# Performance work log

Measured on AMD Instinct MI355X. Metric: run time of the kernel, lower is better.

The kernel has to match this reference:

```python
import jax, jax.numpy as jnp
import numpy as np
from jax import lax

B, T, IN = 32, 512, 32
SNN, TS, HID, HOR = 128, 4, 128, 96
K = 3
THR = 1.0
EPS = 1e-5


def _spike(x):
    # heaviside: fires when (mem - threshold) > 0
    return (x > 0).astype(x.dtype)


def _lif_scan(xs, beta, thr):
    """snntorch Leaky (reset_mechanism='subtract'): mem_t = beta*mem_{t-1} + x_t - spk_{t-1}*thr; spk_t = H(mem_t - thr).
    xs: (S, B, C); beta: (C,). Returns spikes (S,B,C) and membrane (S,B,C)."""
    def step(carry, x):
        mem, rst = carry
        mem = beta * mem + x - rst * thr
        spk = _spike(mem - thr)
        return (mem, lax.stop_gradient(spk)), (spk, mem)
    z = jnp.zeros(xs.shape[1:], xs.dtype)
    _, (spks, mems) = lax.scan(step, (z, z), xs)
    return spks, mems


def setup_inputs() -> dict:
    key = jax.random.key(0)
    ks = jax.random.split(key, 10)
    def rn(k, shape, scale=0.05):
        return jax.random.normal(k, shape, dtype=jnp.float32) * scale
    return {
        "x": jax.random.normal(ks[0], (B, T, IN), dtype=jnp.float32),
        "conv_w": rn(ks[1], (SNN * TS, IN, K)),
        "conv_b": jnp.zeros((SNN * TS,), jnp.float32),
        "bn1_g": jnp.ones((SNN * TS,), jnp.float32),
        "bn1_b": jnp.zeros((SNN * TS,), jnp.float32),
        "beta1": jnp.full((SNN,), 0.9, jnp.float32),
        "bn2_g": jnp.ones((SNN,), jnp.float32),
        "bn2_b": jnp.zeros((SNN,), jnp.float32),
        "beta2": jnp.full((SNN,), 0.9, jnp.float32),
        "gru_wih": rn(ks[2], (3 * HID, IN + SNN)),
        "gru_whh": rn(ks[3], (3 * HID, HID)),
        "gru_bih": jnp.zeros((3 * HID,), jnp.float32),
        "gru_bhh": jnp.zeros((3 * HID,), jnp.float32),
        "q_w": rn(ks[4], (HID, HID)), "q_b": jnp.zeros((HID,), jnp.float32),
        "k_w": rn(ks[5], (HID, HID)), "k_b": jnp.zeros((HID,), jnp.float32),
        "v_w": rn(ks[6], (HID, HID)), "v_b": jnp.zeros((HID,), jnp.float32),
        "bn3_g": jnp.ones((HID,), jnp.float32),
        "bn3_b": jnp.zeros((HID,), jnp.float32),
        "head_w": rn(ks[7], (HOR, HID)),
        "head_b": jnp.zeros((HOR,), jnp.float32),
    }


def reference(x, conv_w, conv_b, bn1_g, bn1_b, beta1, bn2_g, bn2_b, beta2,
              gru_wih, gru_whh, gru_bih, gru_bhh, q_w, q_b, k_w, k_b, v_w, v_b,
              bn3_g, bn3_b, head_w, head_b):
    beta1 = jnp.clip(beta1, 0.0, 0.99)
    beta2 = jnp.clip(beta2, 0.0, 0.99)
    # --- ConvSpikeEncoder: Conv1d -> BatchNorm1d (training stats) -> LIF scan ---
    h = lax.conv_general_dilated(x.transpose(0, 2, 1), conv_w, (1,), [(K // 2, K // 2)],
                                 dimension_numbers=('NCH', 'OIH', 'NCH'))
    h = h + conv_b[None, :, None]  # (B, SNN*TS, T)
    m = h.mean((0, 2), keepdims=True)
    v = jnp.var(h, (0, 2), keepdims=True)
    h = (h - m) * lax.rsqrt(v + EPS) * bn1_g[None, :, None] + bn1_b[None, :, None]
    # (B, SNN*TS, T) -> (T*TS, B, SNN), step index = t*TS + s
    h = h.transpose(0, 2, 1).reshape(B, T * TS, SNN).transpose(1, 0, 2)
    spk_enc, _ = _lif_scan(h, beta1, THR)  # (T*TS, B, SNN)
    # --- per-step BatchNorm1d over batch dim, then second LIF ---
    m2 = spk_enc.mean(1, keepdims=True)
    v2 = jnp.var(spk_enc, 1, keepdims=True)
    h2 = (spk_enc - m2) * lax.rsqrt(v2 + EPS) * bn2_g + bn2_b
    _, mem_rec = _lif_scan(h2, beta2, THR)  # (T*TS, B, SNN)
    # --- downsample membrane: mean over TS sub-steps ---
    mem_down = mem_rec.transpose(1, 0, 2).reshape(B, T, TS, SNN).mean(2)  # (B, T, SNN)
    hc = jnp.concatenate([x, mem_down], -1)  # (B, T, IN+SNN)
    # --- GRU (PyTorch gate order r,z,n) ---
    def gstep(hprev, xt):
        gi = xt @ gru_wih.T + gru_bih
        gh = hprev @ gru_whh.T + gru_bhh
        ir, iz, inn = jnp.split(gi, 3, -1)
        hr, hz, hn = jnp.split(gh, 3, -1)
        r = jax.nn.sigmoid(ir + hr)
        zg = jax.nn.sigmoid(iz + hz)
        n = jnp.tanh(inn + r * hn)
        hnew = (1.0 - zg) * n + zg * hprev
        return hnew, hnew
    _, gru_seq = lax.scan(gstep, jnp.zeros((B, HID), x.dtype), hc.transpose(1, 0, 2))
    g = gru_seq.transpose(1, 0, 2)  # (B, T, HID)
    # --- SpikingAttention: sigmoid(QK^T*scale) @ V, mean over T, BatchNorm ---
    Q = g @ q_w.T + q_b
    Kk = g @ k_w.T + k_b
    V = g @ v_w.T + v_b
    attn = jax.nn.sigmoid(jnp.einsum('btc,bsc->bts', Q, Kk) * (HID ** -0.5))
    out = jnp.einsum('bts,bsc->btc', attn, V).mean(1)  # (B, HID)
    m3 = out.mean(0, keepdims=True)
    v3 = jnp.var(out, 0, keepdims=True)
    out = (out - m3) * lax.rsqrt(v3 + EPS) * bn3_g + bn3_b
    return out @ head_w.T + head_b  # (B, HOR)
```

## Files before the change

kernel.cpp:

```cpp
#include <hip/hip_runtime.h>
#include <math.h>

#define EPSV 1e-5f

#if __has_builtin(__builtin_amdgcn_exp2f)
#define EXP2F(x) __builtin_amdgcn_exp2f(x)
#else
#define EXP2F(x) exp2f(x)
#endif
#if __has_builtin(__builtin_amdgcn_rcpf)
#define RCPF(x) __builtin_amdgcn_rcpf(x)
#else
#define RCPF(x) (1.0f/(x))
#endif

__device__ __forceinline__ float fsigmoid(float x){
  return RCPF(1.0f + EXP2F(-1.4426950408889634f * x));
}
__device__ __forceinline__ float ftanh(float x){
  return RCPF(0.5f + 0.5f * EXP2F(-2.8853900817779268f * x)) - 1.0f;
}
__device__ __forceinline__ unsigned short f2bf(float f){
  unsigned u = __float_as_uint(f);
  return (unsigned short)((u + 0x7FFFu + ((u >> 16) & 1u)) >> 16);
}

typedef __attribute__((ext_vector_type(8))) short bf16x8;
typedef __attribute__((ext_vector_type(8))) short s16x8;
typedef __attribute__((ext_vector_type(4))) float f32x4;
typedef __attribute__((ext_vector_type(2))) _Float16 f16x2;
typedef __attribute__((ext_vector_type(8))) _Float16 f16x8;

#if __has_builtin(__builtin_amdgcn_fdot2)
#define FDOT2(a,b,c) __builtin_amdgcn_fdot2(a,b,c,false)
#else
__device__ __forceinline__ float FDOT2(f16x2 a, f16x2 b, float c){
  return c + (float)a[0]*(float)b[0] + (float)a[1]*(float)b[1];
}
#endif

__device__ __forceinline__ float dot8(f16x8 w, f16x8 h, float acc){
  f16x2 w0 = {w[0],w[1]}, w1 = {w[2],w[3]}, w2 = {w[4],w[5]}, w3 = {w[6],w[7]};
  f16x2 h0 = {h[0],h[1]}, h1 = {h[2],h[3]}, h2 = {h[4],h[5]}, h3 = {h[6],h[7]};
  acc = FDOT2(w0,h0,acc); acc = FDOT2(w1,h1,acc);
  acc = FDOT2(w2,h2,acc); acc = FDOT2(w3,h3,acc);
  return acc;
}

__global__ __launch_bounds__(256) void k_conv(const float* __restrict__ x, const float* __restrict__ w,
        const float* __restrict__ cb, float* __restrict__ hp, float* __restrict__ s1g, float* __restrict__ s2g,
        unsigned short* __restrict__ x_bf){
  __shared__ float xs[32*321];
  __shared__ float ws[32*97];
  __shared__ float bs[32];
  const int tid = threadIdx.x;
  const int t0 = blockIdx.x * 8;
  const int n0 = blockIdx.y * 8;
  for (int idx = tid; idx < 32*10*32; idx += 256){
    int bq = idx / 320; int rem = idx - bq*320; int tt = rem >> 5; int i = rem & 31;
    int tg = t0 - 1 + tt;
    float v = 0.f;
    if (tg >= 0 && tg < 512) v = x[(bq*512 + tg)*32 + i];
    xs[bq*321 + tt*32 + i] = v;
  }
  for (int idx = tid; idx < 32*96; idx += 256){
    int row = idx / 96; int within = idx - row*96;
    int ss = row >> 3; int nl = row & 7;
    int c = ss*128 + n0 + nl;
    ws[row*97 + within] = w[c*96 + within];
  }
  if (tid < 32){
    int ss = tid >> 3, nl = tid & 7;
    bs[tid] = cb[ss*128 + n0 + nl];
  }
  __syncthreads();
  if (blockIdx.y == 0){
    for (int idx = tid; idx < 32*8*32; idx += 256){
      int bq = idx >> 8; int rem = idx & 255; int tt = rem >> 5; int i = rem & 31;
      x_bf[(bq*512 + t0 + tt)*32 + i] = f2bf(xs[bq*321 + (tt+1)*32 + i]);
    }
  }
  const int b = tid & 31;
  const int nl = tid >> 5;
  float acc[4][8];
  #pragma unroll
  for (int ss = 0; ss < 4; ++ss){
    float bv = bs[ss*8 + nl];
    #pragma unroll
    for (int t = 0; t < 8; ++t) acc[ss][t] = bv;
  }
  for (int i = 0; i < 32; ++i){
    #pragma unroll
    for (int k = 0; k < 3; ++k){
      float w0 = ws[(0*8+nl)*97 + i*3 + k];
      float w1 = ws[(1*8+nl)*97 + i*3 + k];
      float w2 = ws[(2*8+nl)*97 + i*3 + k];
      float w3 = ws[(3*8+nl)*97 + i*3 + k];
      #pragma unroll
      for (int t = 0; t < 8; ++t){
        float xv = xs[b*321 + (t+k)*32 + i];
        acc[0][t] += xv*w0; acc[1][t] += xv*w1; acc[2][t] += xv*w2; acc[3][t] += xv*w3;
      }
    }
  }
  #pragma unroll
  for (int ss = 0; ss < 4; ++ss){
    int n = n0 + nl;
    float s1 = 0.f, s2 = 0.f;
    #pragma unroll
    for (int t = 0; t < 8; ++t){
      float v = acc[ss][t];
      int s = (t0 + t)*4 + ss;
      hp[s*4096 + n*32 + b] = v;
      s1 += v; s2 += v*v;
    }
    #pragma unroll
    for (int off = 1; off < 32; off <<= 1){
      s1 += __shfl_xor(s1, off);
      s2 += __shfl_xor(s2, off);
    }
    if (b == 0){
      int c = ss*128 + n;
      atomicAdd(&s1g[c], s1);
      atomicAdd(&s2g[c], s2);
    }
  }
}

__global__ void k_bn1(const float* __restrict__ s1g, const float* __restrict__ s2g,
                      const float* __restrict__ g, const float* __restrict__ bb,
                      float* __restrict__ a1, float* __restrict__ b1){
  int c = threadIdx.x;
  float m = s1g[c] * (1.f/16384.f);
  float v = s2g[c] * (1.f/16384.f) - m*m;
  float sc = g[c] * rsqrtf(v + EPSV);
  a1[c] = sc;
  b1[c] = bb[c] - m*sc;
}

__global__ __launch_bounds__(256) void k_cvt_all(const float* __restrict__ wih,
        const float* __restrict__ qw, const float* __restrict__ kw, const float* __restrict__ vw,
        const float* __restrict__ whh,
        unsigned short* __restrict__ wih_bf, unsigned short* __restrict__ wqkv_bf,
        _Float16* __restrict__ whh_h){
  int i = blockIdx.x*256 + threadIdx.x;
  if (i < 61440){ wih_bf[i] = f2bf(wih[i]); return; }
  int r = i - 61440;
  if (r < 16384){ wqkv_bf[r] = f2bf(qw[r]); return; }
  r -= 16384;
  if (r < 16384){ wqkv_bf[16384 + r] = f2bf(kw[r]); return; }
  r -= 16384;
  if (r < 16384){ wqkv_bf[32768 + r] = f2bf(vw[r]); return; }
  r -= 16384;
  if (r < 49152){ whh_h[r] = (_Float16)whh[r]; }
}

__global__ __launch_bounds__(256) void k_lif(const float* __restrict__ hp,
        const float* __restrict__ a1, const float* __restrict__ b1,
        const float* __restrict__ beta1, const float* __restrict__ g2v, const float* __restrict__ b2v,
        const float* __restrict__ beta2, unsigned short* __restrict__ md_t){
  const int tid = threadIdx.x;
  const int b = tid & 31;
  const int n = blockIdx.x * 8 + (tid >> 5);
  float a1r0 = a1[0*128+n], a1r1 = a1[1*128+n], a1r2 = a1[2*128+n], a1r3 = a1[3*128+n];
  float b1r0 = b1[0*128+n], b1r1 = b1[1*128+n], b1r2 = b1[2*128+n], b1r3 = b1[3*128+n];
  float be1 = fminf(fmaxf(beta1[n], 0.f), 0.99f);
  float be2 = fminf(fmaxf(beta2[n], 0.f), 0.99f);
  float g2 = g2v[n], bb2 = b2v[n];
  float m1 = 0.f, r1 = 0.f, m2 = 0.f, r2 = 0.f;
  const float* base = hp + n*32 + b;
  float c0 = base[0], c1 = base[4096], c2 = base[2*4096], c3 = base[3*4096];
  const float* nb1 = base + 16384;
  float d0 = nb1[0], d1 = nb1[4096], d2 = nb1[2*4096], d3 = nb1[3*4096];

#define LIF_STEP(CV, A1R, B1R) { \
    float x1 = CV*A1R + B1R; \
    m1 = be1*m1 + x1 - r1; \
    bool sp = (m1 > 1.0f); \
    unsigned long long mk = __ballot(sp); \
    float spk = sp ? 1.f : 0.f; r1 = spk; \
    unsigned hf = (tid & 32) ? (unsigned)(mk >> 32) : (unsigned)mk; \
    float mean = (float)__popc(hf) * 0.03125f; \
    float var = mean - mean*mean; \
    float h2 = (spk - mean) * rsqrtf(var + EPSV) * g2 + bb2; \
    m2 = be2*m2 + h2 - r2; \
    r2 = (m2 > 1.0f) ? 1.f : 0.f; \
    accd += m2; }

  for (int t = 0; t < 512; ++t){
    float e0 = 0.f, e1 = 0.f, e2 = 0.f, e3 = 0.f;
    if (t < 510){
      const float* nb = base + (size_t)(t+2)*16384;
      e0 = nb[0]; e1 = nb[4096]; e2 = nb[2*4096]; e3 = nb[3*4096];
    }
    float accd = 0.f;
    LIF_STEP(c0, a1r0, b1r0)
    LIF_STEP(c1, a1r1, b1r1)
    LIF_STEP(c2, a1r2, b1r2)
    LIF_STEP(c3, a1r3, b1r3)
    md_t[((t*128) + n)*32 + b] = f2bf(accd * 0.25f);
    c0 = d0; c1 = d1; c2 = d2; c3 = d3;
    d0 = e0; d1 = e1; d2 = e2; d3 = e3;
  }
#undef LIF_STEP
}

__global__ __launch_bounds__(256) void k_tr(const unsigned short* __restrict__ md_t,
        unsigned short* __restrict__ md_bf){
  __shared__ unsigned short l[128][40];
  const int t = blockIdx.x;
  const int tid = threadIdx.x;
  const unsigned short* src = md_t + (size_t)t*4096;
  #pragma unroll
  for (int r = 0; r < 2; ++r){
    int idx = tid*16 + r*8;
    s16x8 v = *(const s16x8*)(src + idx);
    int nn = idx >> 5, b0 = idx & 31;
    #pragma unroll
    for (int e = 0; e < 8; ++e) l[nn][b0 + e] = (unsigned short)v[e];
  }
  __syncthreads();
  const int b = tid >> 3, seg = tid & 7;
  unsigned short tmp[16];
  #pragma unroll
  for (int i = 0; i < 16; ++i) tmp[i] = l[seg*16 + i][b];
  unsigned short* dst = md_bf + (size_t)(b*512 + t)*128 + seg*16;
  *(s16x8*)(dst + 0) = *(s16x8*)&tmp[0];
  *(s16x8*)(dst + 8) = *(s16x8*)&tmp[8];
}

__global__ __launch_bounds__(256) void k_mm_gi(const unsigned short* __restrict__ xbf,
        const unsigned short* __restrict__ mdbf, const unsigned short* __restrict__ wihbf,
        const float* __restrict__ bih, float* __restrict__ gi2){
  const int tid = threadIdx.x;
  const int w = tid >> 6, l = tid & 63;
  const int c16 = l & 15, kg = l >> 4;
  const int m0 = (blockIdx.x*4 + w) * 16;
  const int mrow = m0 + c16;
  bf16x8 a0 = *(const bf16x8*)&xbf[(size_t)mrow*32 + kg*8];
  const unsigned short* mdp = &mdbf[(size_t)mrow*128 + kg*8];
  bf16x8 a1 = *(const bf16x8*)(mdp + 0);
  bf16x8 a2 = *(const bf16x8*)(mdp + 32);
  bf16x8 a3 = *(const bf16x8*)(mdp + 64);
  bf16x8 a4 = *(const bf16x8*)(mdp + 96);
  for (int nt = 0; nt < 24; ++nt){
    int n0 = nt*16;
    const unsigned short* wp = &wihbf[(size_t)(n0 + c16)*160 + kg*8];
    bf16x8 b0 = *(const bf16x8*)(wp + 0);
    bf16x8 b1 = *(const bf16x8*)(wp + 32);
    bf16x8 b2 = *(const bf16x8*)(wp + 64);
    bf16x8 b3 = *(const bf16x8*)(wp + 96);
    bf16x8 b4 = *(const bf16x8*)(wp + 128);
    f32x4 acc = {0.f,0.f,0.f,0.f};
    acc = __builtin_amdgcn_mfma_f32_16x16x32_bf16(a0, b0, acc, 0, 0, 0);
    acc = __builtin_amdgcn_mfma_f32_16x16x32_bf16(a1, b1, acc, 0, 0, 0);
    acc = __builtin_amdgcn_mfma_f32_16x16x32_bf16(a2, b2, acc, 0, 0, 0);
    acc = __builtin_amdgcn_mfma_f32_16x16x32_bf16(a3, b3, acc, 0, 0, 0);
    acc = __builtin_amdgcn_mfma_f32_16x16x32_bf16(a4, b4, acc, 0, 0, 0);
    int n = n0 + c16;
    int gate = n >> 7;
    int jj = n & 127;
    float bias = bih[n];
    #pragma unroll
    for (int r = 0; r < 4; ++r){
      gi2[(size_t)(m0 + kg*4 + r)*512 + jj*4 + gate] = acc[r] + bias;
    }
  }
}

template<int SEL>
__device__ __forceinline__ float dpp_qp(float x){
  return __int_as_float(__builtin_amdgcn_mov_dpp(__float_as_int(x), SEL, 0xF, 0xF, true));
}
__device__ __forceinline__ float qbc(float x, int u){
  switch(u){
    case 0: return dpp_qp<0x00>(x);
    case 1: return dpp_qp<0x55>(x);
    case 2: return dpp_qp<0xAA>(x);
    default: return dpp_qp<0xFF>(x);
  }
}
__global__ __launch_bounds__(512, 2) void k_gru(const float* __restrict__ gi2, const _Float16* __restrict__ whh_h,
        const float* __restrict__ bhh, unsigned short* __restrict__ gout_bf){
  const int b = blockIdx.x;
  const int tid = threadIdx.x;
  const int j = tid >> 2;
  const int q = tid & 3;
  __shared__ _Float16 hs[2][144];
  const _Float16* wbr = whh_h + (size_t)(      j)*128 + q*32;
  const _Float16* wbz = whh_h + (size_t)(128 + j)*128 + q*32;
  const _Float16* wbn = whh_h + (size_t)(256 + j)*128 + q*32;
  f16x8 wr0 = *(const f16x8*)(wbr+ 0), wr1 = *(const f16x8*)(wbr+ 8),
        wr2 = *(const f16x8*)(wbr+16), wr3 = *(const f16x8*)(wbr+24);
  f16x8 wz0 = *(const f16x8*)(wbz+ 0), wz1 = *(const f16x8*)(wbz+ 8),
        wz2 = *(const f16x8*)(wbz+16), wz3 = *(const f16x8*)(wbz+24);
  f16x8 wn0 = *(const f16x8*)(wbn+ 0), wn1 = *(const f16x8*)(wbn+ 8),
        wn2 = *(const f16x8*)(wbn+16), wn3 = *(const f16x8*)(wbn+24);
  float bh_r = 0.f, bh_z = 0.f, bh_n = 0.f;
  if (!q){
    bh_r = bhh[j]; bh_z = bhh[128+j]; bh_n = bhh[256+j];
  }
  const float* gib = gi2 + (size_t)b*512*512;
  f32x4 G = *(const f32x4*)(gib + (size_t)q*512 + j*4);
  if (tid < 128) hs[0][tid] = (_Float16)0.f;
  float hprev = 0.f;
  __syncthreads();
  for (int g = 0; g < 128; ++g){
    f32x4 N = {0.f,0.f,0.f,0.f};
    if (g < 127) N = *(const f32x4*)(gib + (size_t)(4*(g+1) + q)*512 + j*4);
    #pragma unroll
    for (int u = 0; u < 4; ++u){
      const int t = g*4 + u;
      float gr = qbc(G[0], u);
      float gz = qbc(G[1], u);
      float gn = qbc(G[2], u);
      const f16x8* hq = (const f16x8*)&hs[t & 1][q*32];
      f16x8 h0 = hq[0], h1 = hq[1], h2 = hq[2], h3 = hq[3];
      float ar = 0.f, az = 0.f, an = 0.f;
      ar = dot8(wr0,h0,ar); ar = dot8(wr1,h1,ar); ar = dot8(wr2,h2,ar); ar = dot8(wr3,h3,ar);
      az = dot8(wz0,h0,az); az = dot8(wz1,h1,az); az = dot8(wz2,h2,az); az = dot8(wz3,h3,az);
      an = dot8(wn0,h0,an); an = dot8(wn1,h1,an); an = dot8(wn2,h2,an); an = dot8(wn3,h3,an);
      ar += dpp_qp<0xB1>(ar); ar += dpp_qp<0x4E>(ar);
      az += dpp_qp<0xB1>(az); az += dpp_qp<0x4E>(az);
      an += dpp_qp<0xB1>(an); an += dpp_qp<0x4E>(an);
      if (!q){
        float r = fsigmoid(gr + ar + bh_r);
        float z = fsigmoid(gz + az + bh_z);
        float nn = ftanh(gn + r*(an + bh_n));
        float hn = (1.f - z)*nn + z*hprev;
        hprev = hn;
        hs[(t + 1) & 1][j] = (_Float16)hn;
        gout_bf[((size_t)b*512 + t)*128 + j] = f2bf(hn);
      }
      __syncthreads();
    }
    G = N;
  }
}

__global__ __launch_bounds__(256) void k_mm_qkv(const unsigned short* __restrict__ gbf,
        const unsigned short* __restrict__ wbf, const float* __restrict__ qb2,
        const float* __restrict__ kb2, const float* __restrict__ vb2,
        unsigned short* __restrict__ Qbf, unsigned short* __restrict__ Kbf, float* __restrict__ Vb){
  const int tid = threadIdx.x;
  const int w = tid >> 6, l = tid & 63;
  const int c16 = l & 15, kg = l >> 4;
  const int m0 = (blockIdx.x*4 + w) * 16;
  const unsigned short* gp = &gbf[(size_t)(m0 + c16)*128 + kg*8];
  bf16x8 a0 = *(const bf16x8*)(gp + 0);
  bf16x8 a1 = *(const bf16x8*)(gp + 32);
  bf16x8 a2 = *(const bf16x8*)(gp + 64);
  bf16x8 a3 = *(const bf16x8*)(gp + 96);
  for (int nt = 0; nt < 24; ++nt){
    int n0 = nt*16;
    const unsigned short* wp = &wbf[(size_t)(n0 + c16)*128 + kg*8];
    bf16x8 b0 = *(const bf16x8*)(wp + 0);
    bf16x8 b1 = *(const bf16x8*)(wp + 32);
    bf16x8 b2 = *(const bf16x8*)(wp + 64);
    bf16x8 b3 = *(const bf16x8*)(wp + 96);
    f32x4 acc = {0.f,0.f,0.f,0.f};
    acc = __builtin_amdgcn_mfma_f32_16x16x32_bf16(a0, b0, acc, 0, 0, 0);
    acc = __builtin_amdgcn_mfma_f32_16x16x32_bf16(a1, b1, acc, 0, 0, 0);
    acc = __builtin_amdgcn_mfma_f32_16x16x32_bf16(a2, b2, acc, 0, 0, 0);
    acc = __builtin_amdgcn_mfma_f32_16x16x32_bf16(a3, b3, acc, 0, 0, 0);
    int n = n0 + c16;
    if (n < 128){
      float bias = qb2[n];
      #pragma unroll
      for (int r = 0; r < 4; ++r)
        Qbf[(size_t)(m0 + kg*4 + r)*128 + n] = f2bf(acc[r] + bias);
    } else if (n < 256){
      float bias = kb2[n-128];
      #pragma unroll
      for (int r = 0; r < 4; ++r)
        Kbf[(size_t)(m0 + kg*4 + r)*128 + (n-128)] = f2bf(acc[r] + bias);
    } else {
      float bias = vb2[n-256];
      #pragma unroll
      for (int r = 0; r < 4; ++r)
        Vb[(size_t)(m0 + kg*4 + r)*128 + (n-256)] = acc[r] + bias;
    }
  }
}

__global__ __launch_bounds__(256) void k_attn(const unsigned short* __restrict__ Qbf,
        const unsigned short* __restrict__ Kbf, float* __restrict__ av){
  const int tid = threadIdx.x;
  const int b  = blockIdx.x;
  const int st = blockIdx.y;
  const int w  = tid >> 6;
  const int l  = tid & 63;
  const int c16 = l & 15;
  const int kg  = l >> 4;
  const float SC = 0.08838834764831845f;
  const unsigned short* kp = Kbf + ((size_t)(b*512 + st*64 + w*16 + c16))*128 + kg*8;
  bf16x8 a0 = *(const bf16x8*)(kp + 0);
  bf16x8 a1 = *(const bf16x8*)(kp + 32);
  bf16x8 a2 = *(const bf16x8*)(kp + 64);
  bf16x8 a3 = *(const bf16x8*)(kp + 96);
  const unsigned short* qb = Qbf + ((size_t)(b*512 + c16))*128 + kg*8;
  float ps0 = 0.f, ps1 = 0.f, ps2 = 0.f, ps3 = 0.f;
  for (int tt = 0; tt < 32; ++tt){
    const unsigned short* qp = qb + (size_t)tt*16*128;
    bf16x8 b0 = *(const bf16x8*)(qp + 0);
    bf16x8 b1 = *(const bf16x8*)(qp + 32);
    bf16x8 b2 = *(const bf16x8*)(qp + 64);
    bf16x8 b3 = *(const bf16x8*)(qp + 96);
    f32x4 acc = {0.f, 0.f, 0.f, 0.f};
    acc = __builtin_amdgcn_mfma_f32_16x16x32_bf16(a0, b0, acc, 0, 0, 0);
    acc = __builtin_amdgcn_mfma_f32_16x16x32_bf16(a1, b1, acc, 0, 0, 0);
    acc = __builtin_amdgcn_mfma_f32_16x16x32_bf16(a2, b2, acc, 0, 0, 0);
    acc = __builtin_amdgcn_mfma_f32_16x16x32_bf16(a3, b3, acc, 0, 0, 0);
    ps0 += fsigmoid(acc[0]*SC);
    ps1 += fsigmoid(acc[1]*SC);
    ps2 += fsigmoid(acc[2]*SC);
    ps3 += fsigmoid(acc[3]*SC);
  }
  #pragma unroll
  for (int off = 1; off < 16; off <<= 1){
    ps0 += __shfl_xor(ps0, off);
    ps1 += __shfl_xor(ps1, off);
    ps2 += __shfl_xor(ps2, off);
    ps3 += __shfl_xor(ps3, off);
  }
  if (c16 == 0){
    int sb = st*64 + w*16 + kg*4;
    av[b*512 + sb + 0] = ps0 * (1.f/512.f);
    av[b*512 + sb + 1] = ps1 * (1.f/512.f);
    av[b*512 + sb + 2] = ps2 * (1.f/512.f);
    av[b*512 + sb + 3] = ps3 * (1.f/512.f);
  }
}

__global__ __launch_bounds__(128) void k_av(const float* __restrict__ av, const float* __restrict__ Vb,
        float* __restrict__ out0){
  int b = blockIdx.x, c = threadIdx.x;
  float a0 = 0.f, a1 = 0.f, a2 = 0.f, a3 = 0.f;
  for (int s = 0; s < 512; s += 4){
    a0 += av[b*512 + s+0] * Vb[(size_t)(b*512 + s+0)*128 + c];
    a1 += av[b*512 + s+1] * Vb[(size_t)(b*512 + s+1)*128 + c];
    a2 += av[b*512 + s+2] * Vb[(size_t)(b*512 + s+2)*128 + c];
    a3 += av[b*512 + s+3] * Vb[(size_t)(b*512 + s+3)*128 + c];
  }
  out0[b*128 + c] = (a0 + a1) + (a2 + a3);
}

__global__ __launch_bounds__(256) void k_final(const float* __restrict__ out0,
        const float* __restrict__ g3, const float* __restrict__ b3,
        const float* __restrict__ hw, const float* __restrict__ hb, float* __restrict__ out){
  __shared__ float on[32*132];
  const int tid = threadIdx.x;
  if (tid < 128){
    int c = tid;
    float s = 0.f;
    for (int bq = 0; bq < 32; ++bq) s += out0[bq*128 + c];
    float m = s * (1.f/32.f);
    float v = 0.f;
    for (int bq = 0; bq < 32; ++bq){ float d = out0[bq*128 + c] - m; v += d*d; }
    v *= (1.f/32.f);
    float sc = g3[c] * rsqrtf(v + EPSV);
    float sh = b3[c] - m*sc;
    for (int bq = 0; bq < 32; ++bq) on[bq*132 + c] = out0[bq*128 + c]*sc + sh;
  }
  __syncthreads();
  for (int o = tid; o < 32*96; o += 256){
    int bq = o / 96, hh = o - bq*96;
    float acc = hb[hh];
    for (int k = 0; k < 128; ++k) acc += on[bq*132 + k] * hw[hh*128 + k];
    out[o] = acc;
  }
}

extern "C" void kernel_launch(void* const* d_in, const int* in_sizes, int n_in,
                              void* d_out, int out_size, void* d_ws, size_t ws_size,
                              hipStream_t stream){
  const float* x      = (const float*)d_in[0];
  const float* conv_w = (const float*)d_in[1];
  const float* conv_b = (const float*)d_in[2];
  const float* bn1_g  = (const float*)d_in[3];
  const float* bn1_b  = (const float*)d_in[4];
  const float* beta1  = (const float*)d_in[5];
  const float* bn2_g  = (const float*)d_in[6];
  const float* bn2_b  = (const float*)d_in[7];
  const float* beta2  = (const float*)d_in[8];
  const float* g_wih  = (const float*)d_in[9];
  const float* g_whh  = (const float*)d_in[10];
  const float* g_bih  = (const float*)d_in[11];
  const float* g_bhh  = (const float*)d_in[12];
  const float* q_w    = (const float*)d_in[13];
  const float* q_b    = (const float*)d_in[14];
  const float* k_w    = (const float*)d_in[15];
  const float* k_b    = (const float*)d_in[16];
  const float* v_w    = (const float*)d_in[17];
  const float* v_b    = (const float*)d_in[18];
  const float* bn3_g  = (const float*)d_in[19];
  const float* bn3_b  = (const float*)d_in[20];
  const float* head_w = (const float*)d_in[21];
  const float* head_b = (const float*)d_in[22];

  char* ws = (char*)d_ws;
  float* hp            = (float*)ws;
  unsigned short* md_bf= (unsigned short*)(ws + 33554432);
  unsigned short* md_t = (unsigned short*)(ws + 37748736);
  unsigned short* g_bf = (unsigned short*)(ws + 37748736);
  unsigned short* x_bf = (unsigned short*)(ws + 41943040);
  unsigned short* wih_bf  = (unsigned short*)(ws + 42991616);
  unsigned short* wqkv_bf = (unsigned short*)(ws + 43114496);
  _Float16* whh_h      = (_Float16*)(ws + 43212800);
  float* s1g = (float*)(ws + 50331648);
  float* s2g = (float*)(ws + 50331648 + 2048);
  float* a1  = (float*)(ws + 50331648 + 4096);
  float* b1  = (float*)(ws + 50331648 + 6144);
  float* av  = (float*)(ws + 50331648 + 8192);
  float* out0= (float*)(ws + 50331648 + 8192 + 65536);
  float* gi2 = (float*)ws;
  unsigned short* Qbf = (unsigned short*)ws;
  unsigned short* Kbf = (unsigned short*)(ws + 4194304);
  float* Vb  = (float*)(ws + 8388608);

  (void)hipMemsetAsync(ws + 50331648, 0, 4096, stream);

  k_conv<<<dim3(64, 16), 256, 0, stream>>>(x, conv_w, conv_b, hp, s1g, s2g, x_bf);
  k_bn1<<<1, 512, 0, stream>>>(s1g, s2g, bn1_g, bn1_b, a1, b1);
  k_cvt_all<<<624, 256, 0, stream>>>(g_wih, q_w, k_w, v_w, g_whh, wih_bf, wqkv_bf, whh_h);
  k_lif<<<16, 256, 0, stream>>>(hp, a1, b1, beta1, bn2_g, bn2_b, beta2, md_t);
  k_tr<<<512, 256, 0, stream>>>(md_t, md_bf);
  k_mm_gi<<<256, 256, 0, stream>>>(x_bf, md_bf, wih_bf, g_bih, gi2);
  k_gru<<<32, 512, 0, stream>>>(gi2, whh_h, g_bhh, g_bf);
  k_mm_qkv<<<256, 256, 0, stream>>>(g_bf, wqkv_bf, q_b, k_b, v_b, Qbf, Kbf, Vb);
  k_attn<<<dim3(32, 8), 256, 0, stream>>>(Qbf, Kbf, av);
  k_av<<<32, 128, 0, stream>>>(av, Vb, out0);
  k_final<<<1, 256, 0, stream>>>(out0, bn3_g, bn3_b, head_w, head_b, (float*)d_out);
}
```

Baseline: 635.0 us.

## Fuse BN1 finalize into weight convert, vectorize gate stores, deepen GRU prefetch

Folds the BN1 scale/shift computation into two extra blocks of the weight-conversion kernel, which removes one kernel launch. The GI matmul now computes r/z/n gates together per column tile and writes them as one float4 instead of scattered scalar stores. The GRU kernel prefetches input-gate data two groups ahead instead of one, to hide global load latency in the serial recurrence. The risks are extra register pressure in the GRU and the matmul, and the float4 store also writes the unused fourth slot.

```diff
diff --git a/kernel.cpp b/kernel.cpp
--- a/kernel.cpp
+++ b/kernel.cpp
@@ -127,22 +127,25 @@
   }
 }
 
-__global__ void k_bn1(const float* __restrict__ s1g, const float* __restrict__ s2g,
-                      const float* __restrict__ g, const float* __restrict__ bb,
-                      float* __restrict__ a1, float* __restrict__ b1){
-  int c = threadIdx.x;
-  float m = s1g[c] * (1.f/16384.f);
-  float v = s2g[c] * (1.f/16384.f) - m*m;
-  float sc = g[c] * rsqrtf(v + EPSV);
-  a1[c] = sc;
-  b1[c] = bb[c] - m*sc;
-}
-
 __global__ __launch_bounds__(256) void k_cvt_all(const float* __restrict__ wih,
         const float* __restrict__ qw, const float* __restrict__ kw, const float* __restrict__ vw,
         const float* __restrict__ whh,
         unsigned short* __restrict__ wih_bf, unsigned short* __restrict__ wqkv_bf,
-        _Float16* __restrict__ whh_h){
+        _Float16* __restrict__ whh_h,
+        const float* __restrict__ s1g, const float* __restrict__ s2g,
+        const float* __restrict__ g, const float* __restrict__ bb,
+        float* __restrict__ a1, float* __restrict__ b1){
+  if (blockIdx.x >= 624){
+    int c = (blockIdx.x - 624)*256 + threadIdx.x;
+    if (c < 512){
+      float m = s1g[c] * (1.f/16384.f);
+      float v = s2g[c] * (1.f/16384.f) - m*m;
+      float sc = g[c] * rsqrtf(v + EPSV);
+      a1[c] = sc;
+      b1[c] = bb[c] - m*sc;
+    }
+    return;
+  }
   int i = blockIdx.x*256 + threadIdx.x;
   if (i < 61440){ wih_bf[i] = f2bf(wih[i]); return; }
   int r = i - 61440;
@@ -243,27 +246,28 @@
   bf16x8 a2 = *(const bf16x8*)(mdp + 32);
   bf16x8 a3 = *(const bf16x8*)(mdp + 64);
   bf16x8 a4 = *(const bf16x8*)(mdp + 96);
-  for (int nt = 0; nt < 24; ++nt){
-    int n0 = nt*16;
-    const unsigned short* wp = &wihbf[(size_t)(n0 + c16)*160 + kg*8];
-    bf16x8 b0 = *(const bf16x8*)(wp + 0);
-    bf16x8 b1 = *(const bf16x8*)(wp + 32);
-    bf16x8 b2 = *(const bf16x8*)(wp + 64);
-    bf16x8 b3 = *(const bf16x8*)(wp + 96);
-    bf16x8 b4 = *(const bf16x8*)(wp + 128);
-    f32x4 acc = {0.f,0.f,0.f,0.f};
-    acc = __builtin_amdgcn_mfma_f32_16x16x32_bf16(a0, b0, acc, 0, 0, 0);
-    acc = __builtin_amdgcn_mfma_f32_16x16x32_bf16(a1, b1, acc, 0, 0, 0);
-    acc = __builtin_amdgcn_mfma_f32_16x16x32_bf16(a2, b2, acc, 0, 0, 0);
-    acc = __builtin_amdgcn_mfma_f32_16x16x32_bf16(a3, b3, acc, 0, 0, 0);
-    acc = __builtin_amdgcn_mfma_f32_16x16x32_bf16(a4, b4, acc, 0, 0, 0);
-    int n = n0 + c16;
-    int gate = n >> 7;
-    int jj = n & 127;
-    float bias = bih[n];
+  for (int nt2 = 0; nt2 < 8; ++nt2){
+    int n0 = nt2*16;
+    const unsigned short* wr = &wihbf[(size_t)(      n0 + c16)*160 + kg*8];
+    const unsigned short* wz = &wihbf[(size_t)(128 + n0 + c16)*160 + kg*8];
+    const unsigned short* wn = &wihbf[(size_t)(256 + n0 + c16)*160 + kg*8];
+    f32x4 ar = {0.f,0.f,0.f,0.f}, az = {0.f,0.f,0.f,0.f}, an = {0.f,0.f,0.f,0.f};
+    #pragma unroll
+    for (int c = 0; c < 5; ++c){
+      bf16x8 br = *(const bf16x8*)(wr + c*32);
+      bf16x8 bz = *(const bf16x8*)(wz + c*32);
+      bf16x8 bn = *(const bf16x8*)(wn + c*32);
+      bf16x8 aa = (c == 0) ? a0 : (c == 1) ? a1 : (c == 2) ? a2 : (c == 3) ? a3 : a4;
+      ar = __builtin_amdgcn_mfma_f32_16x16x32_bf16(aa, br, ar, 0, 0, 0);
+      az = __builtin_amdgcn_mfma_f32_16x16x32_bf16(aa, bz, az, 0, 0, 0);
+      an = __builtin_amdgcn_mfma_f32_16x16x32_bf16(aa, bn, an, 0, 0, 0);
+    }
+    float br_ = bih[n0 + c16], bz_ = bih[128 + n0 + c16], bn_ = bih[256 + n0 + c16];
+    int jj = n0 + c16;
     #pragma unroll
     for (int r = 0; r < 4; ++r){
-      gi2[(size_t)(m0 + kg*4 + r)*512 + jj*4 + gate] = acc[r] + bias;
+      float4 o = { ar[r] + br_, az[r] + bz_, an[r] + bn_, 0.f };
+      *(float4*)&gi2[(size_t)(m0 + kg*4 + r)*512 + jj*4] = o;
     }
   }
 }
@@ -302,12 +306,13 @@
   }
   const float* gib = gi2 + (size_t)b*512*512;
   f32x4 G = *(const f32x4*)(gib + (size_t)q*512 + j*4);
+  f32x4 N = *(const f32x4*)(gib + (size_t)(4 + q)*512 + j*4);
   if (tid < 128) hs[0][tid] = (_Float16)0.f;
   float hprev = 0.f;
   __syncthreads();
   for (int g = 0; g < 128; ++g){
-    f32x4 N = {0.f,0.f,0.f,0.f};
-    if (g < 127) N = *(const f32x4*)(gib + (size_t)(4*(g+1) + q)*512 + j*4);
+    f32x4 N2 = {0.f,0.f,0.f,0.f};
+    if (g < 126) N2 = *(const f32x4*)(gib + (size_t)(4*(g+2) + q)*512 + j*4);
     #pragma unroll
     for (int u = 0; u < 4; ++u){
       const int t = g*4 + u;
@@ -334,7 +339,7 @@
       }
       __syncthreads();
     }
-    G = N;
+    G = N; N = N2;
   }
 }
 
@@ -521,8 +526,8 @@
   (void)hipMemsetAsync(ws + 50331648, 0, 4096, stream);
 
   k_conv<<<dim3(64, 16), 256, 0, stream>>>(x, conv_w, conv_b, hp, s1g, s2g, x_bf);
-  k_bn1<<<1, 512, 0, stream>>>(s1g, s2g, bn1_g, bn1_b, a1, b1);
-  k_cvt_all<<<624, 256, 0, stream>>>(g_wih, q_w, k_w, v_w, g_whh, wih_bf, wqkv_bf, whh_h);
+  k_cvt_all<<<626, 256, 0, stream>>>(g_wih, q_w, k_w, v_w, g_whh, wih_bf, wqkv_bf, whh_h,
+                                     s1g, s2g, bn1_g, bn1_b, a1, b1);
   k_lif<<<16, 256, 0, stream>>>(hp, a1, b1, beta1, bn2_g, bn2_b, beta2, md_t);
   k_tr<<<512, 256, 0, stream>>>(md_t, md_bf);
   k_mm_gi<<<256, 256, 0, stream>>>(x_bf, md_bf, wih_bf, g_bih, gi2);
```

Result: faster. 615.2 us (-3.1%).
